# Performance work log

Measured on AMD Instinct MI355X. Metric: run time of the kernel, lower is better.

The kernel has to match this reference:

```python
import jax, jax.numpy as jnp
import numpy as np


def qdq(x):
    """Per-tensor symmetric int8 quantize-dequantize (act_quant + fp8_gemm dequant semantics)."""
    scale = jnp.maximum(jnp.max(jnp.abs(x)) / 127.0, 1e-8)
    q = jnp.clip(jnp.round(x / scale), -127.0, 127.0) * scale
    # straight-through estimator so the reference is also usable under autodiff
    return x + jax.lax.stop_gradient(q - x)


def layernorm(x, scale, bias, eps=1e-6):
    mean = jnp.mean(x, axis=-1, keepdims=True)
    var = jnp.mean(jnp.square(x - mean), axis=-1, keepdims=True)
    return (x - mean) * jax.lax.rsqrt(var + eps) * scale + bias


def glin(t, W, b):
    """TPUGEMMLinear: quantized GEMM (dequantized matmul) + bias."""
    return jnp.matmul(qdq(t), qdq(W)) + b


def setup_inputs() -> dict:
    key = jax.random.key(0)
    ks = jax.random.split(key, 12)
    B, S, D = 4, 1024, 1024
    H, HD, F, P = 32, 32, 4096, 32
    lecun = lambda k, shape: jax.random.normal(k, shape, jnp.float32) * (1.0 / np.sqrt(shape[0]))
    return {
        'inputs': jax.random.normal(ks[0], (B, S, D), jnp.float32),
        'ln1_scale': jnp.ones((D,), jnp.float32),
        'ln1_bias': jnp.zeros((D,), jnp.float32),
        'Wq': lecun(ks[1], (D, H * HD)), 'bq': jnp.zeros((H * HD,), jnp.float32),
        'Wk': lecun(ks[2], (D, H * HD)), 'bk': jnp.zeros((H * HD,), jnp.float32),
        'Wv': lecun(ks[3], (D, H * HD)), 'bv': jnp.zeros((H * HD,), jnp.float32),
        'rel_pos_emb': jax.random.normal(ks[4], (2 * P + 1, HD), jnp.float32) * 0.02,
        'Wo': lecun(ks[5], (H * HD, D)), 'bo': jnp.zeros((D,), jnp.float32),
        'ln2_scale': jnp.ones((D,), jnp.float32),
        'ln2_bias': jnp.zeros((D,), jnp.float32),
        'W1': lecun(ks[6], (D, F)), 'b1': jnp.zeros((F,), jnp.float32),
        'W2': lecun(ks[7], (F, D)), 'b2': jnp.zeros((D,), jnp.float32),
    }


def reference(inputs, ln1_scale, ln1_bias, Wq, bq, Wk, bk, Wv, bv, rel_pos_emb,
              Wo, bo, ln2_scale, ln2_bias, W1, b1, W2, b2):
    B, S, D = inputs.shape
    HD = rel_pos_emb.shape[1]
    H = D // HD
    P = (rel_pos_emb.shape[0] - 1) // 2

    # Pre-attention LayerNorm (TPULayerNorm, eps=1e-6)
    x = layernorm(inputs, ln1_scale, ln1_bias)

    # Quantized QKV projections
    q = glin(x, Wq, bq).reshape(B, S, H, HD).transpose(0, 2, 1, 3)  # [B,H,S,HD]
    k = glin(x, Wk, bk).reshape(B, S, H, HD).transpose(0, 2, 1, 3)
    v = glin(x, Wv, bv).reshape(B, S, H, HD).transpose(0, 2, 1, 3)

    # Relative position bias: [1, HD, S, S] broadcast onto head axis (HD == H by construction)
    pos = jnp.clip(jnp.arange(S)[:, None] - jnp.arange(S)[None, :] + P, 0, 2 * P)
    rel_bias = rel_pos_emb[pos].transpose(2, 0, 1)[None]  # [1, HD, S, S]

    # Quantized content scores + bias, custom scale factor
    scores = jnp.einsum('bhqd,bhkd->bhqk', qdq(q), qdq(k)) + rel_bias
    scale = jnp.sqrt(jnp.asarray(HD, jnp.float32)) * jnp.power(jnp.asarray(S, jnp.float32), 0.25)
    scores = scores / scale

    # Stable softmax with +1e-6 denominator (as in source)
    m = jnp.max(scores, axis=-1, keepdims=True)
    e = jnp.exp(scores - m)
    w = e / (jnp.sum(e, axis=-1, keepdims=True) + 1e-6)

    attn = jnp.einsum('bhqk,bhkd->bhqd', w, qdq(v))  # values quantized, weights not
    attn = attn.transpose(0, 2, 1, 3).reshape(B, S, H * HD)
    attn_out = glin(attn, Wo, bo)

    xr = attn_out + inputs
    y = layernorm(xr, ln2_scale, ln2_bias)

    # MLP (_mlp_tpu assumed: quantized Linear -> gelu -> quantized Linear)
    h = jax.nn.gelu(glin(y, W1, b1))
    out = glin(h, W2, b2)
    # NOTE: source returns mlp_output directly (no second residual add)
    return out
```

## Files before the change

kernel.cpp:

```cpp
#include <hip/hip_runtime.h>
#include <cstdint>


typedef unsigned short u16;
typedef __bf16 bf16x4 __attribute__((ext_vector_type(4)));
typedef __bf16 bf16x8 __attribute__((ext_vector_type(8)));
typedef float  f32x4  __attribute__((ext_vector_type(4)));

#define MFMA(a, b, c) __builtin_amdgcn_mfma_f32_16x16x32_bf16(a, b, c, 0, 0, 0)

#define NSLOT 13
#define PSPREAD 64
#define PSTRIDE 16
#define SLOTSZ (PSPREAD * PSTRIDE)

__device__ __forceinline__ float bf2f(u16 h) {
    return __uint_as_float(((unsigned)h) << 16);
}
__device__ __forceinline__ u16 f2bf(float f) {
    unsigned u = __float_as_uint(f);
    u += 0x7FFFu + ((u >> 16) & 1u);
    return (u16)(u >> 16);
}
__device__ __forceinline__ float qdqv(float v, float s) {
    float q = rintf(v / s);
    q = fminf(fmaxf(q, -127.f), 127.f);
    return q * s;
}

__device__ __forceinline__ float getscale64(const int* scales, int slot) {
    float m = __int_as_float(scales[slot * SLOTSZ + (threadIdx.x & 63) * PSTRIDE]);
#pragma unroll
    for (int o = 32; o > 0; o >>= 1) m = fmaxf(m, __shfl_xor(m, o));
    return fmaxf(m / 127.f, 1e-8f);
}

typedef const __attribute__((address_space(1))) unsigned gas_u32;
typedef __attribute__((address_space(3))) unsigned las_u32;
__device__ __forceinline__ void gld16(const void* g, void* l) {
    __builtin_amdgcn_global_load_lds((gas_u32*)g, (las_u32*)l, 16, 0, 0);
}

__global__ void zero_k(int* s) {
    const int i = blockIdx.x * 256 + threadIdx.x;
    if (i < NSLOT * SLOTSZ) s[i] = 0;
}

__device__ __forceinline__ float blk_sum(float v, float* red) {
#pragma unroll
    for (int o = 32; o > 0; o >>= 1) v += __shfl_xor(v, o);
    __syncthreads();
    if ((threadIdx.x & 63) == 0) red[threadIdx.x >> 6] = v;
    __syncthreads();
    return red[0] + red[1] + red[2] + red[3];
}

__device__ __forceinline__ void blk_absmax_commit(float am, float* red, int* scales,
                                                  int slot, int bidx) {
#pragma unroll
    for (int o = 32; o > 0; o >>= 1) am = fmaxf(am, __shfl_xor(am, o));
    __syncthreads();
    if ((threadIdx.x & 63) == 0) red[threadIdx.x >> 6] = am;
    __syncthreads();
    if (threadIdx.x == 0) {
        float m = fmaxf(fmaxf(red[0], red[1]), fmaxf(red[2], red[3]));
        atomicMax(scales + slot * SLOTSZ + ((bidx & (PSPREAD - 1)) * PSTRIDE),
                  __float_as_int(m));
    }
}

__global__ __launch_bounds__(256) void waln_k(const float* __restrict__ w0, const float* __restrict__ w1,
                                              const float* __restrict__ w2, const float* __restrict__ w3,
                                              const float* __restrict__ w4, const float* __restrict__ w5,
                                              const float* __restrict__ in, const float* __restrict__ gam,
                                              const float* __restrict__ bet, u16* __restrict__ out,
                                              int* __restrict__ scales) {
    __shared__ float red[4];
    const int tid = threadIdx.x;
    if (blockIdx.x < 3072) {
        const int b = blockIdx.x;
        int ti, boff;
        if (b < 1024)      { ti = b >> 8; boff = (b & 255) * 4096; }
        else if (b < 2048) { ti = 4;      boff = (b - 1024) * 4096; }
        else               { ti = 5;      boff = (b - 2048) * 4096; }
        const float* w = (ti == 0) ? w0 : (ti == 1) ? w1 : (ti == 2) ? w2
                       : (ti == 3) ? w3 : (ti == 4) ? w4 : w5;
        const float4* wv = (const float4*)(w + boff);
        float m = 0.f;
#pragma unroll
        for (int k = 0; k < 4; k++) {
            float4 v = wv[tid + k * 256];
            m = fmaxf(m, fmaxf(fmaxf(fabsf(v.x), fabsf(v.y)), fmaxf(fabsf(v.z), fabsf(v.w))));
        }
#pragma unroll
        for (int o = 32; o > 0; o >>= 1) m = fmaxf(m, __shfl_xor(m, o));
        if ((tid & 63) == 0)
            atomicMax(scales + (7 + ti) * SLOTSZ + (((b * 4 + (tid >> 6)) & (PSPREAD - 1)) * PSTRIDE),
                      __float_as_int(m));
        return;
    }
    const long row = blockIdx.x - 3072;
    float4 v = ((const float4*)(in + row * 1024))[tid];
    float mean = blk_sum(v.x + v.y + v.z + v.w, red) * (1.f / 1024.f);
    float dx = v.x - mean, dy = v.y - mean, dz = v.z - mean, dw = v.w - mean;
    float var = blk_sum(dx * dx + dy * dy + dz * dz + dw * dw, red) * (1.f / 1024.f);
    float inv = rsqrtf(var + 1e-6f);
    float4 gg = ((const float4*)gam)[tid];
    float4 bb = ((const float4*)bet)[tid];
    float o0 = dx * inv * gg.x + bb.x, o1 = dy * inv * gg.y + bb.y;
    float o2 = dz * inv * gg.z + bb.z, o3 = dw * inv * gg.w + bb.w;
    ushort4 st;
    st.x = f2bf(o0); st.y = f2bf(o1); st.z = f2bf(o2); st.w = f2bf(o3);
    ((ushort4*)(out + row * 1024))[tid] = st;
    float am = fmaxf(fmaxf(fabsf(o0), fabsf(o1)), fmaxf(fabsf(o2), fabsf(o3)));
    blk_absmax_commit(am, red, scales, 0, (int)row);
}

__global__ __launch_bounds__(256) void wqt6_k(const float* __restrict__ w0, const float* __restrict__ w1,
                                              const float* __restrict__ w2, const float* __restrict__ w3,
                                              const float* __restrict__ w4, const float* __restrict__ w5,
                                              u16* __restrict__ wtbase, const int* __restrict__ scales) {
    __shared__ float t[32][33];
    const int b = blockIdx.x;
    const float* W;
    u16* Wt;
    int K, N, bx, by, slot;
    if (b < 4096) {
        const int ti = b >> 10, r = b & 1023;
        W = (ti == 0) ? w0 : (ti == 1) ? w1 : (ti == 2) ? w2 : w3;
        Wt = wtbase + (long)ti * 1048576;
        K = 1024; N = 1024; bx = r & 31; by = r >> 5; slot = 7 + ti;
    } else if (b < 8192) {
        const int r = b - 4096;
        W = w4; Wt = wtbase + 4194304;
        K = 1024; N = 4096; bx = r & 127; by = r >> 7; slot = 11;
    } else {
        const int r = b - 8192;
        W = w5; Wt = wtbase + 8388608;
        K = 4096; N = 1024; bx = r & 31; by = r >> 5; slot = 12;
    }
    const int n0 = bx * 32, k0 = by * 32;
    const float s = getscale64(scales, slot);
    const int c = threadIdx.x & 31, r0 = threadIdx.x >> 5;
#pragma unroll
    for (int i = 0; i < 4; i++) {
        int kk = k0 + r0 + i * 8;
        t[r0 + i * 8][c] = qdqv(W[(long)kk * N + n0 + c], s);
    }
    __syncthreads();
#pragma unroll
    for (int i = 0; i < 4; i++) {
        int nn = n0 + r0 + i * 8;
        Wt[(long)nn * K + k0 + c] = f2bf(t[c][r0 + i * 8]);
    }
}

__global__ __launch_bounds__(256) void ln2comb_k(const float* __restrict__ p, const float* __restrict__ bo,
                                                 const float* __restrict__ inputs,
                                                 const float* __restrict__ gam, const float* __restrict__ bet,
                                                 u16* __restrict__ out, int* __restrict__ scales) {
    __shared__ float red[4];
    const long row = blockIdx.x;
    const int tid = threadIdx.x;
    float4 a = ((const float4*)(p + row * 1024))[tid];
    float4 b = ((const float4*)(p + 4194304 + row * 1024))[tid];
    float4 bb0 = ((const float4*)bo)[tid];
    float4 xi = ((const float4*)(inputs + row * 1024))[tid];
    float4 v;
    v.x = a.x + b.x + bb0.x + xi.x; v.y = a.y + b.y + bb0.y + xi.y;
    v.z = a.z + b.z + bb0.z + xi.z; v.w = a.w + b.w + bb0.w + xi.w;
    float mean = blk_sum(v.x + v.y + v.z + v.w, red) * (1.f / 1024.f);
    float dx = v.x - mean, dy = v.y - mean, dz = v.z - mean, dw = v.w - mean;
    float var = blk_sum(dx * dx + dy * dy + dz * dz + dw * dw, red) * (1.f / 1024.f);
    float inv = rsqrtf(var + 1e-6f);
    float4 gg = ((const float4*)gam)[tid];
    float4 bb = ((const float4*)bet)[tid];
    float o0 = dx * inv * gg.x + bb.x, o1 = dy * inv * gg.y + bb.y;
    float o2 = dz * inv * gg.z + bb.z, o3 = dw * inv * gg.w + bb.w;
    ushort4 st;
    st.x = f2bf(o0); st.y = f2bf(o1); st.z = f2bf(o2); st.w = f2bf(o3);
    ((ushort4*)(out + row * 1024))[tid] = st;
    float am = fmaxf(fmaxf(fabsf(o0), fabsf(o1)), fmaxf(fabsf(o2), fabsf(o3)));
    blk_absmax_commit(am, red, scales, 5, (int)row);
}

__global__ void combo_k(const float* __restrict__ pa, const float* __restrict__ pc,
                        const float* __restrict__ b2, float* __restrict__ out) {
    const int i = blockIdx.x * 256 + threadIdx.x;
    float4 a0 = ((const float4*)pa)[i];
    float4 a1 = ((const float4*)(pa + 4194304))[i];
    float4 c0 = ((const float4*)pc)[i];
    float4 c1 = ((const float4*)out)[i];
    float4 bb = ((const float4*)b2)[i & 255];
    float4 o;
    o.x = ((a0.x + a1.x) + (c0.x + c1.x)) + bb.x;
    o.y = ((a0.y + a1.y) + (c0.y + c1.y)) + bb.y;
    o.z = ((a0.z + a1.z) + (c0.z + c1.z)) + bb.z;
    o.w = ((a0.w + a1.w) + (c0.w + c1.w)) + bb.w;
    ((float4*)out)[i] = o;
}

__global__ void qact_k(u16* buf, int n8, const int* __restrict__ scales, int slot) {
    const float s = getscale64(scales, slot);
    int i = blockIdx.x * 256 + threadIdx.x;
    if (i >= n8) return;
    uint4 u = ((const uint4*)buf)[i];
    unsigned w[4] = {u.x, u.y, u.z, u.w};
#pragma unroll
    for (int j = 0; j < 4; j++) {
        float lo = qdqv(bf2f((u16)(w[j] & 0xFFFFu)), s);
        float hi = qdqv(bf2f((u16)(w[j] >> 16)), s);
        w[j] = (unsigned)f2bf(lo) | ((unsigned)f2bf(hi) << 16);
    }
    uint4 o; o.x = w[0]; o.y = w[1]; o.z = w[2]; o.w = w[3];
    ((uint4*)buf)[i] = o;
}

__global__ __launch_bounds__(256) void vq_k(u16* __restrict__ qk, const u16* __restrict__ v,
                                            u16* __restrict__ vt, const int* __restrict__ scales) {
    __shared__ u16 t[32][33];
    const int tid = threadIdx.x;
    if (blockIdx.x < 4096) {
        const int i = blockIdx.x * 256 + tid;
        const int slot = (i >= 524288) ? 2 : 1;
        const float s = getscale64(scales, slot);
        uint4 u = ((const uint4*)qk)[i];
        unsigned w[4] = {u.x, u.y, u.z, u.w};
#pragma unroll
        for (int j = 0; j < 4; j++) {
            float lo = qdqv(bf2f((u16)(w[j] & 0xFFFFu)), s);
            float hi = qdqv(bf2f((u16)(w[j] >> 16)), s);
            w[j] = (unsigned)f2bf(lo) | ((unsigned)f2bf(hi) << 16);
        }
        uint4 o; o.x = w[0]; o.y = w[1]; o.z = w[2]; o.w = w[3];
        ((uint4*)qk)[i] = o;
        return;
    }
    const int r = blockIdx.x - 4096;
    const int bh = r >> 5, s0 = (r & 31) * 32;
    const float s = getscale64(scales, 3);
    const int c = tid & 31, r0 = tid >> 5;
    const u16* src = v + ((long)bh * 1024 + s0) * 32;
#pragma unroll
    for (int i = 0; i < 4; i++) {
        int rr = r0 + i * 8;
        t[rr][c] = f2bf(qdqv(bf2f(src[rr * 32 + c]), s));
    }
    __syncthreads();
    u16* dst = vt + (long)bh * 32768;
#pragma unroll
    for (int i = 0; i < 4; i++) {
        int rr = r0 + i * 8;
        dst[(long)rr * 1024 + s0 + c] = t[c][rr];
    }
}

template <int EPI>
__global__ __launch_bounds__(256, 2) void gemm_k(const u16* __restrict__ A, const u16* __restrict__ Bt,
                                                 const float* __restrict__ bias, const float* __restrict__ bias2,
                                                 const float* __restrict__ bias3,
                                                 int M, int N, int Kfull, int Kslice,
                                                 float* __restrict__ outf, float* __restrict__ outf2,
                                                 float* __restrict__ outf3, u16* __restrict__ outb,
                                                 int* __restrict__ scales, int slot) {
    __shared__ u16 As[128 * 64];
    __shared__ u16 Bs[128 * 64];
    const float* bp = bias;
    long koff = 0, ooff = 0;
    float* po = outf;
    if (EPI == 0) {
        const int z = blockIdx.z;
        Bt += (long)z * 1048576;
        outb += (long)z * 4194304;
        bp = (z == 0) ? bias : (z == 1 ? bias2 : bias3);
        slot += z;
    }
    if (EPI == 4) {
        const int z = blockIdx.z;
        koff = (long)z * Kslice * 2;
        if (z < 2)       { po = outf;  ooff = (long)z * M * N; }
        else if (z == 2) { po = outf2; ooff = 0; }
        else             { po = outf3; ooff = 0; }
    }
    const int tid = threadIdx.x;
    const int lane = tid & 63;
    const int wave = tid >> 6;
    const int wm = wave >> 1, wn = wave & 1;
    const int bm = blockIdx.y * 128, bn = blockIdx.x * 128;
    const int g = lane >> 4, c = lane & 15;

    const long astride = (long)Kfull * 2;
    const int srow = wave * 32 + (lane >> 3);
    const int scol = ((lane & 7) * 16) ^ ((lane >> 3) << 4);
    const char* Ag = (const char*)A + (long)(bm + srow) * astride + scol + koff;
    const char* Bg = (const char*)Bt + (long)(bn + srow) * astride + scol + koff;
    char* Al = (char*)As + wave * 4096;
    char* Bl = (char*)Bs + wave * 4096;

    f32x4 acc[4][4];
    const f32x4 zf = {0.f, 0.f, 0.f, 0.f};
#pragma unroll
    for (int i = 0; i < 4; i++)
#pragma unroll
        for (int j = 0; j < 4; j++) acc[i][j] = zf;

    const int nk = Kslice >> 6;
    for (int kt = 0; kt < nk; ++kt) {
        __syncthreads();
        const long ko = (long)kt * 128;
#pragma unroll
        for (int i = 0; i < 4; i++) gld16(Ag + ko + (long)(i * 8) * astride, Al + i * 1024);
#pragma unroll
        for (int i = 0; i < 4; i++) gld16(Bg + ko + (long)(i * 8) * astride, Bl + i * 1024);
        __syncthreads();

#pragma unroll
        for (int kh = 0; kh < 2; kh++) {
            bf16x8 af[4], bq[4];
            const int kb = kh * 64 + g * 16;
            const int sw = kb ^ ((c & 7) << 4);
#pragma unroll
            for (int i = 0; i < 4; i++)
                af[i] = *(const bf16x8*)((const char*)As + (wm * 64 + i * 16 + c) * 128 + sw);
#pragma unroll
            for (int j = 0; j < 4; j++)
                bq[j] = *(const bf16x8*)((const char*)Bs + (wn * 64 + j * 16 + c) * 128 + sw);
#pragma unroll
            for (int i = 0; i < 4; i++)
#pragma unroll
                for (int j = 0; j < 4; j++)
                    acc[i][j] = MFMA(af[i], bq[j], acc[i][j]);
        }
    }

    float am = 0.f;
#pragma unroll
    for (int i = 0; i < 4; i++) {
#pragma unroll
        for (int j = 0; j < 4; j++) {
#pragma unroll
            for (int t = 0; t < 4; t++) {
                const int row = bm + wm * 64 + i * 16 + g * 4 + t;
                const int col = bn + wn * 64 + j * 16 + c;
                if (EPI == 0) {
                    float v = acc[i][j][t] + bp[col];
                    long oi = ((long)((row >> 10) * 32 + (col >> 5))) * 32768
                              + (long)(row & 1023) * 32 + (col & 31);
                    outb[oi] = f2bf(v);
                    am = fmaxf(am, fabsf(v));
                } else if (EPI == 2) {
                    float v = acc[i][j][t] + bp[col];
                    float t3 = v * v * v;
                    float gl = 0.5f * v * (1.f + tanhf(0.79788456080286536f * (v + 0.044715f * t3)));
                    outb[(long)row * N + col] = f2bf(gl);
                    am = fmaxf(am, fabsf(gl));
                } else {
                    po[ooff + (long)row * N + col] = acc[i][j][t];
                }
            }
        }
    }
    if (EPI == 0 || EPI == 2) {
#pragma unroll
        for (int o = 32; o > 0; o >>= 1) am = fmaxf(am, __shfl_xor(am, o));
        if (lane == 0)
            atomicMax(scales + slot * SLOTSZ
                          + ((((blockIdx.x + blockIdx.y * gridDim.x) * 4 + wave) & (PSPREAD - 1)) * PSTRIDE),
                      __float_as_int(am));
    }
}

__global__ __launch_bounds__(256) void attn_k(const u16* __restrict__ q, const u16* __restrict__ k,
                                              const u16* __restrict__ vt, const float* __restrict__ relpos,
                                              u16* __restrict__ attn, int* __restrict__ scales) {
    __shared__ float rel_s[65];
    __shared__ __align__(16) u16 P[4][32 * 40];
    __shared__ float frs[4][32];
    const int tid = threadIdx.x;
    const int lane = tid & 63;
    const int w = tid >> 6;
    const int bh = blockIdx.x;
    const int b = bh >> 5, h = bh & 31;
    const int q0 = blockIdx.y * 128 + w * 32;
    const int g = lane >> 4, c = lane & 15;
    const float SC = 0.03125f;
    for (int i = tid; i < 65; i += 256) rel_s[i] = relpos[i * 32 + h] * SC;
    __syncthreads();
    const float rb0 = rel_s[0], rb64 = rel_s[64];

    const u16* qb = q + ((long)bh * 1024 + q0) * 32;
    const u16* kb = k + (long)bh * 32768;
    const u16* vb = vt + (long)bh * 32768;
    u16* Pw = P[w];
    float* fw = frs[w];

    bf16x8 aq[2];
#pragma unroll
    for (int i = 0; i < 2; i++) aq[i] = *(const bf16x8*)(qb + (i * 16 + c) * 32 + g * 8);

    const f32x4 zf = {0.f, 0.f, 0.f, 0.f};
    f32x4 o[2][2] = {{zf, zf}, {zf, zf}};
    float m_run[2] = {-1e30f, -1e30f};
    float l_run[2] = {0.f, 0.f};

    bf16x8 bk0 = *(const bf16x8*)(kb + (0 + c) * 32 + g * 8);
    bf16x8 bk1 = *(const bf16x8*)(kb + (16 + c) * 32 + g * 8);
    bf16x8 bv0 = *(const bf16x8*)(vb + c * 1024 + 0 + g * 8);
    bf16x8 bv1 = *(const bf16x8*)(vb + (16 + c) * 1024 + 0 + g * 8);

    for (int kt = 0; kt < 32; ++kt) {
        const int kk = kt * 32;
        const int kkn = ((kt + 1) & 31) * 32;
        bf16x8 nk0 = *(const bf16x8*)(kb + (kkn + c) * 32 + g * 8);
        bf16x8 nk1 = *(const bf16x8*)(kb + (kkn + 16 + c) * 32 + g * 8);
        bf16x8 nv0 = *(const bf16x8*)(vb + c * 1024 + kkn + g * 8);
        bf16x8 nv1 = *(const bf16x8*)(vb + (16 + c) * 1024 + kkn + g * 8);

        const int mode = (kk >= q0 + 64) ? 0 : (kk <= q0 - 64) ? 1 : 2;
        float frv[2];
#pragma unroll
        for (int i = 0; i < 2; i++) {
            f32x4 s0 = MFMA(bk0, aq[i], zf);
            f32x4 s1 = MFMA(bk1, aq[i], zf);
            float v[8];
            if (mode == 0) {
#pragma unroll
                for (int t = 0; t < 4; t++) { v[t] = fmaf(s0[t], SC, rb0); v[4 + t] = fmaf(s1[t], SC, rb0); }
            } else if (mode == 1) {
#pragma unroll
                for (int t = 0; t < 4; t++) { v[t] = fmaf(s0[t], SC, rb64); v[4 + t] = fmaf(s1[t], SC, rb64); }
            } else {
                const int base = (q0 + i * 16 + c) - kk - g * 4 + 32;
#pragma unroll
                for (int t = 0; t < 4; t++) {
                    int d0 = min(max(base - t, 0), 64);
                    int d1 = min(max(base - 16 - t, 0), 64);
                    v[t] = fmaf(s0[t], SC, rel_s[d0]);
                    v[4 + t] = fmaf(s1[t], SC, rel_s[d1]);
                }
            }
            float mt = fmaxf(fmaxf(fmaxf(v[0], v[1]), fmaxf(v[2], v[3])),
                             fmaxf(fmaxf(v[4], v[5]), fmaxf(v[6], v[7])));
            mt = fmaxf(mt, __shfl_xor(mt, 16));
            mt = fmaxf(mt, __shfl_xor(mt, 32));
            const float mn = fmaxf(m_run[i], mt);
            const float fr = __expf(m_run[i] - mn);
            frv[i] = fr;
            float sm = 0.f;
            bf16x4 pk0, pk1;
#pragma unroll
            for (int t = 0; t < 4; t++) {
                float p = __expf(v[t] - mn);     sm += p; pk0[t] = (__bf16)p;
                float p2 = __expf(v[4 + t] - mn); sm += p2; pk1[t] = (__bf16)p2;
            }
            sm += __shfl_xor(sm, 16);
            sm += __shfl_xor(sm, 32);
            l_run[i] = l_run[i] * fr + sm;
            m_run[i] = mn;
            *(bf16x4*)&Pw[(i * 16 + c) * 40 + g * 4] = pk0;
            *(bf16x4*)&Pw[(i * 16 + c) * 40 + 16 + g * 4] = pk1;
        }
        if (__any((frv[0] != 1.f) | (frv[1] != 1.f))) {
            if (g == 0) { fw[c] = frv[0]; fw[16 + c] = frv[1]; }
            float4 f0 = *(float4*)&fw[g * 4];
            float4 f1 = *(float4*)&fw[16 + g * 4];
#pragma unroll
            for (int j = 0; j < 2; j++) {
                o[0][j][0] *= f0.x; o[0][j][1] *= f0.y; o[0][j][2] *= f0.z; o[0][j][3] *= f0.w;
                o[1][j][0] *= f1.x; o[1][j][1] *= f1.y; o[1][j][2] *= f1.z; o[1][j][3] *= f1.w;
            }
        }
        bf16x8 ap0 = *(const bf16x8*)&Pw[c * 40 + g * 8];
        bf16x8 ap1 = *(const bf16x8*)&Pw[(16 + c) * 40 + g * 8];
        o[0][0] = MFMA(ap0, bv0, o[0][0]);
        o[0][1] = MFMA(ap0, bv1, o[0][1]);
        o[1][0] = MFMA(ap1, bv0, o[1][0]);
        o[1][1] = MFMA(ap1, bv1, o[1][1]);
        bk0 = nk0; bk1 = nk1; bv0 = nv0; bv1 = nv1;
    }

    if (g == 0) { fw[c] = l_run[0]; fw[16 + c] = l_run[1]; }
    float4 l0 = *(float4*)&fw[g * 4];
    float4 l1 = *(float4*)&fw[16 + g * 4];
    float lv[2][4] = {{l0.x, l0.y, l0.z, l0.w}, {l1.x, l1.y, l1.z, l1.w}};
    float am = 0.f;
#pragma unroll
    for (int i = 0; i < 2; i++)
#pragma unroll
        for (int j = 0; j < 2; j++)
#pragma unroll
            for (int t = 0; t < 4; t++) {
                float val = o[i][j][t] / (lv[i][t] + 1e-6f);
                long row = (long)b * 1024 + q0 + i * 16 + g * 4 + t;
                attn[row * 1024 + h * 32 + j * 16 + c] = f2bf(val);
                am = fmaxf(am, fabsf(val));
            }
#pragma unroll
    for (int o2 = 32; o2 > 0; o2 >>= 1) am = fmaxf(am, __shfl_xor(am, o2));
    if (lane == 0)
        atomicMax(scales + 4 * SLOTSZ + ((((bh * 8 + blockIdx.y) * 4 + w) & (PSPREAD - 1)) * PSTRIDE),
                  __float_as_int(am));
}

extern "C" void kernel_launch(void* const* d_in, const int* in_sizes, int n_in,
                              void* d_out, int out_size, void* d_ws, size_t ws_size,
                              hipStream_t stream) {
    (void)in_sizes; (void)n_in; (void)out_size; (void)ws_size;
    const float* inputs = (const float*)d_in[0];
    const float* ln1s   = (const float*)d_in[1];
    const float* ln1b   = (const float*)d_in[2];
    const float* Wq     = (const float*)d_in[3];
    const float* bq     = (const float*)d_in[4];
    const float* Wk     = (const float*)d_in[5];
    const float* bk     = (const float*)d_in[6];
    const float* Wv     = (const float*)d_in[7];
    const float* bv     = (const float*)d_in[8];
    const float* rel    = (const float*)d_in[9];
    const float* Wo     = (const float*)d_in[10];
    const float* bo     = (const float*)d_in[11];
    const float* ln2s   = (const float*)d_in[12];
    const float* ln2b   = (const float*)d_in[13];
    const float* W1     = (const float*)d_in[14];
    const float* b1     = (const float*)d_in[15];
    const float* W2     = (const float*)d_in[16];
    const float* b2     = (const float*)d_in[17];
    float* out = (float*)d_out;

    char* ws = (char*)d_ws;
    int* scales = (int*)ws;
    char* regionA = ws + 65536;
    char* regionB = regionA + (32u << 20);
    char* regionC = regionB + (32u << 20);
    u16* qb    = (u16*)regionA;
    u16* kbuf  = qb + 4194304;
    u16* vbuf  = kbuf + 4194304;
    u16* vtb   = vbuf + 4194304;
    float* pWo = (float*)regionA;
    u16* hb    = (u16*)regionA;
    u16* xq    = (u16*)regionB;
    u16* attnb = xq;
    u16* yb    = xq + 4194304;
    float* pW2  = (float*)regionB;
    float* pW2c = (float*)regionC;
    u16* wtb   = (u16*)regionC;

    zero_k<<<52, 256, 0, stream>>>(scales);
    waln_k<<<7168, 256, 0, stream>>>(Wq, Wk, Wv, Wo, W1, W2, inputs, ln1s, ln1b, xq, scales);

    wqt6_k<<<12288, 256, 0, stream>>>(Wq, Wk, Wv, Wo, W1, W2, wtb, scales);

    qact_k<<<2048, 256, 0, stream>>>(xq, 524288, scales, 0);

    gemm_k<0><<<dim3(8, 32, 3), 256, 0, stream>>>(xq, wtb, bq, bk, bv, 4096, 1024, 1024, 1024,
                                                  nullptr, nullptr, nullptr, qb, scales, 1);

    vq_k<<<8192, 256, 0, stream>>>(qb, vbuf, vtb, scales);

    attn_k<<<dim3(128, 8), 256, 0, stream>>>(qb, kbuf, vtb, rel, attnb, scales);
    qact_k<<<2048, 256, 0, stream>>>(attnb, 524288, scales, 4);

    gemm_k<4><<<dim3(8, 32, 2), 256, 0, stream>>>(attnb, wtb + 3145728, nullptr, nullptr, nullptr,
                                                  4096, 1024, 1024, 512, pWo, nullptr, nullptr, nullptr,
                                                  scales, -1);
    ln2comb_k<<<4096, 256, 0, stream>>>(pWo, bo, inputs, ln2s, ln2b, yb, scales);
    qact_k<<<2048, 256, 0, stream>>>(yb, 524288, scales, 5);

    gemm_k<2><<<dim3(32, 32), 256, 0, stream>>>(yb, wtb + 4194304, b1, nullptr, nullptr,
                                                4096, 4096, 1024, 1024, nullptr, nullptr, nullptr, hb,
                                                scales, 6);
    qact_k<<<8192, 256, 0, stream>>>(hb, 2097152, scales, 6);

    gemm_k<4><<<dim3(8, 32, 4), 256, 0, stream>>>(hb, wtb + 8388608, nullptr, nullptr, nullptr,
                                                  4096, 1024, 4096, 1024, pW2, pW2c, out, nullptr,
                                                  scales, -1);
    combo_k<<<4096, 256, 0, stream>>>(pW2, pW2c, b2, out);
}
```

Before: 323.9 us.

## Split Wo GEMM K four ways, raise GEMM occupancy, drop attention prefetch

The Wo projection GEMM now splits K into four slices of 256 instead of two of 512, writing partials into four buffers (reusing the output and a spare region), and the LN2 combine kernel sums all four partials. This puts more blocks on the GPU for that GEMM. GEMM launch bounds go from 2 to 4 blocks per CU, which limits registers per thread and risks spills. The attention kernel drops its software prefetch of next-tile K/V, loading them at the top of each iteration instead, which lowers register pressure but exposes load latency.

```diff
diff --git a/kernel.cpp b/kernel.cpp
--- a/kernel.cpp
+++ b/kernel.cpp
@@ -155,7 +155,8 @@
     }
 }
 
-__global__ __launch_bounds__(256) void ln2comb_k(const float* __restrict__ p, const float* __restrict__ bo,
+__global__ __launch_bounds__(256) void ln2comb_k(const float* __restrict__ p, const float* __restrict__ p2,
+                                                 const float* __restrict__ p3, const float* __restrict__ bo,
                                                  const float* __restrict__ inputs,
                                                  const float* __restrict__ gam, const float* __restrict__ bet,
                                                  u16* __restrict__ out, int* __restrict__ scales) {
@@ -164,11 +165,15 @@
     const int tid = threadIdx.x;
     float4 a = ((const float4*)(p + row * 1024))[tid];
     float4 b = ((const float4*)(p + 4194304 + row * 1024))[tid];
+    float4 c2 = ((const float4*)(p2 + row * 1024))[tid];
+    float4 c3 = ((const float4*)(p3 + row * 1024))[tid];
     float4 bb0 = ((const float4*)bo)[tid];
     float4 xi = ((const float4*)(inputs + row * 1024))[tid];
     float4 v;
-    v.x = a.x + b.x + bb0.x + xi.x; v.y = a.y + b.y + bb0.y + xi.y;
-    v.z = a.z + b.z + bb0.z + xi.z; v.w = a.w + b.w + bb0.w + xi.w;
+    v.x = ((a.x + b.x) + (c2.x + c3.x)) + bb0.x + xi.x;
+    v.y = ((a.y + b.y) + (c2.y + c3.y)) + bb0.y + xi.y;
+    v.z = ((a.z + b.z) + (c2.z + c3.z)) + bb0.z + xi.z;
+    v.w = ((a.w + b.w) + (c2.w + c3.w)) + bb0.w + xi.w;
     float mean = blk_sum(v.x + v.y + v.z + v.w, red) * (1.f / 1024.f);
     float dx = v.x - mean, dy = v.y - mean, dz = v.z - mean, dw = v.w - mean;
     float var = blk_sum(dx * dx + dy * dy + dz * dz + dw * dw, red) * (1.f / 1024.f);
@@ -256,7 +261,7 @@
 }
 
 template <int EPI>
-__global__ __launch_bounds__(256, 2) void gemm_k(const u16* __restrict__ A, const u16* __restrict__ Bt,
+__global__ __launch_bounds__(256, 4) void gemm_k(const u16* __restrict__ A, const u16* __restrict__ Bt,
                                                  const float* __restrict__ bias, const float* __restrict__ bias2,
                                                  const float* __restrict__ bias3,
                                                  int M, int N, int Kfull, int Kslice,
@@ -403,20 +408,14 @@
     float m_run[2] = {-1e30f, -1e30f};
     float l_run[2] = {0.f, 0.f};
 
-    bf16x8 bk0 = *(const bf16x8*)(kb + (0 + c) * 32 + g * 8);
-    bf16x8 bk1 = *(const bf16x8*)(kb + (16 + c) * 32 + g * 8);
-    bf16x8 bv0 = *(const bf16x8*)(vb + c * 1024 + 0 + g * 8);
-    bf16x8 bv1 = *(const bf16x8*)(vb + (16 + c) * 1024 + 0 + g * 8);
-
     for (int kt = 0; kt < 32; ++kt) {
         const int kk = kt * 32;
-        const int kkn = ((kt + 1) & 31) * 32;
-        bf16x8 nk0 = *(const bf16x8*)(kb + (kkn + c) * 32 + g * 8);
-        bf16x8 nk1 = *(const bf16x8*)(kb + (kkn + 16 + c) * 32 + g * 8);
-        bf16x8 nv0 = *(const bf16x8*)(vb + c * 1024 + kkn + g * 8);
-        bf16x8 nv1 = *(const bf16x8*)(vb + (16 + c) * 1024 + kkn + g * 8);
-
+        bf16x8 bk0 = *(const bf16x8*)(kb + (kk + c) * 32 + g * 8);
+        bf16x8 bk1 = *(const bf16x8*)(kb + (kk + 16 + c) * 32 + g * 8);
+        bf16x8 bv0 = *(const bf16x8*)(vb + c * 1024 + kk + g * 8);
+        bf16x8 bv1 = *(const bf16x8*)(vb + (16 + c) * 1024 + kk + g * 8);
         const int mode = (kk >= q0 + 64) ? 0 : (kk <= q0 - 64) ? 1 : 2;
+
         float frv[2];
 #pragma unroll
         for (int i = 0; i < 2; i++) {
@@ -476,7 +475,6 @@
         o[0][1] = MFMA(ap0, bv1, o[0][1]);
         o[1][0] = MFMA(ap1, bv0, o[1][0]);
         o[1][1] = MFMA(ap1, bv1, o[1][1]);
-        bk0 = nk0; bk1 = nk1; bv0 = nv0; bv1 = nv1;
     }
 
     if (g == 0) { fw[c] = l_run[0]; fw[16 + c] = l_run[1]; }
@@ -536,6 +534,7 @@
     u16* vbuf  = kbuf + 4194304;
     u16* vtb   = vbuf + 4194304;
     float* pWo = (float*)regionA;
+    float* pWo2 = (float*)(regionB + (16u << 20));
     u16* hb    = (u16*)regionA;
     u16* xq    = (u16*)regionB;
     u16* attnb = xq;
@@ -559,10 +558,10 @@
     attn_k<<<dim3(128, 8), 256, 0, stream>>>(qb, kbuf, vtb, rel, attnb, scales);
     qact_k<<<2048, 256, 0, stream>>>(attnb, 524288, scales, 4);
 
-    gemm_k<4><<<dim3(8, 32, 2), 256, 0, stream>>>(attnb, wtb + 3145728, nullptr, nullptr, nullptr,
-                                                  4096, 1024, 1024, 512, pWo, nullptr, nullptr, nullptr,
+    gemm_k<4><<<dim3(8, 32, 4), 256, 0, stream>>>(attnb, wtb + 3145728, nullptr, nullptr, nullptr,
+                                                  4096, 1024, 1024, 256, pWo, pWo2, out, nullptr,
                                                   scales, -1);
-    ln2comb_k<<<4096, 256, 0, stream>>>(pWo, bo, inputs, ln2s, ln2b, yb, scales);
+    ln2comb_k<<<4096, 256, 0, stream>>>(pWo, pWo2, out, bo, inputs, ln2s, ln2b, yb, scales);
     qact_k<<<2048, 256, 0, stream>>>(yb, 524288, scales, 5);
 
     gemm_k<2><<<dim3(32, 32), 256, 0, stream>>>(yb, wtb + 4194304, b1, nullptr, nullptr,
```

New measurement: 323.1 us. No clear change (-0.2%).
